# Performance work log

Measured on AMD Instinct MI355X. Metric: run time of the kernel, lower is better.

The kernel has to match this reference:

```python
import math
import jax, jax.numpy as jnp
import numpy as np

B, N, D = 4, 2048, 512
H, DV, DO = 8, 64, 512


def setup_inputs() -> dict:
    key = jax.random.key(0)
    ks = jax.random.split(key, 8)
    def xavier(k, shape, fan_in, fan_out):
        a = math.sqrt(6.0 / (fan_in + fan_out))
        return jax.random.uniform(k, shape, jnp.float32, -a, a)
    return {
        "query": jax.random.normal(ks[0], (B, N, D), jnp.float32),
        "key": jax.random.normal(ks[1], (B, N, D), jnp.float32),
        "value": jax.random.normal(ks[2], (B, N, D), jnp.float32),
        "attn_mask": jax.random.randint(ks[3], (N, N), 0, 2, jnp.int32),
        "Wq": xavier(ks[4], (H, D, D), D, D),
        "Wk": xavier(ks[5], (H, D, D), D, D),
        "Wv": xavier(ks[6], (H, D, DV), D, DV),
        "Wo": xavier(ks[7], (H * DV, DO), H * DV, DO),
    }


def reference(query, key, value, attn_mask, Wq, Wk, Wv, Wo):
    b, n, d = query.shape
    h, dv = Wv.shape[0], Wv.shape[2]
    # per-head projections: [b, h, n, d] / [b, h, n, dv]
    Q = jnp.einsum('bnd,hde->bhne', query, Wq)
    K = jnp.einsum('bnd,hde->bhne', key, Wk)
    V = jnp.einsum('bnd,hdv->bhnv', value, Wv)
    # multiplicative mask (1: do not attend -> zeroed score), scaled by sqrt(d)
    keep = (1.0 - attn_mask.astype(jnp.float32))[None, None]  # [1,1,n,n]
    QK = jnp.einsum('bhne,bhme->bhnm', Q, K) * keep / math.sqrt(d)
    attn_weights = QK  # linear_attention=True: skip softmax
    QKV = jnp.einsum('bhnm,bhmv->bhnv', attn_weights, V)  # [b,h,n,dv]
    out = QKV.transpose(0, 2, 1, 3).reshape(b, n, h * dv) @ Wo  # [b,n,do]
    return (out, attn_weights)
```

## Files before the change

### kernel.cpp

```cpp
#include <hip/hip_runtime.h>
#include <hip/hip_bf16.h>

#define DEVFN __device__ __forceinline__

constexpr int Bb = 4, Nn = 2048, Dd = 512, Hh = 8, DVv = 64, DOo = 512;

typedef short short8 __attribute__((ext_vector_type(8)));
typedef float f32x4 __attribute__((ext_vector_type(4)));

typedef __attribute__((address_space(1))) void GV;
typedef __attribute__((address_space(3))) void LV;

DEVFN unsigned short f32_bf16(float f) {
  unsigned u = __builtin_bit_cast(unsigned, f);
  u += 0x7fffu + ((u >> 16) & 1u);
  return (unsigned short)(u >> 16);
}

DEVFN void barrier_raw() {
  asm volatile("" ::: "memory");
  __builtin_amdgcn_s_barrier();
  asm volatile("" ::: "memory");
}

template<int Nv> DEVFN void wait_vmcnt() {
  if constexpr (Nv == 0)      asm volatile("s_waitcnt vmcnt(0)"  ::: "memory");
  else if constexpr (Nv == 6) asm volatile("s_waitcnt vmcnt(6)"  ::: "memory");
  else if constexpr (Nv == 8) asm volatile("s_waitcnt vmcnt(8)"  ::: "memory");
  else static_assert(Nv == 0 || Nv == 6 || Nv == 8, "bad vmcnt");
}
DEVFN void wait_lgkm0() { asm volatile("s_waitcnt lgkmcnt(0)" ::: "memory"); }

template<int ROWBYTES, int TOTAL>
DEVFN void stage_tile(const char* g, int strideBytes, char* lds, int tid) {
#pragma unroll
  for (int off = 0; off < TOTAL; off += 4096) {
    int o   = off + tid * 16;
    int row = o / ROWBYTES;
    int blk = (o >> 4) & ((ROWBYTES >> 4) - 1);
    int sb  = blk ^ (row & 7);
    const char* src = g + (size_t)row * strideBytes + (sb << 4);
    __builtin_amdgcn_global_load_lds((GV*)src, (LV*)(lds + o), 16, 0, 0);
  }
}

template<int ROWBYTES>
DEVFN short8 frag_ld(const char* lds, int row, int kbyte) {
  int blk = kbyte >> 4;
  int sb  = blk ^ (row & 7);
  return *(const short8*)(lds + row * ROWBYTES + (sb << 4));
}

DEVFN f32x4 mfma16(short8 a, short8 b, f32x4 c) {
  return __builtin_amdgcn_mfma_f32_16x16x32_bf16(a, b, c, 0, 0, 0);
}


__global__ void cvt_f32_bf16_kernel(const float* __restrict__ in,
                                    unsigned short* __restrict__ out, int n4) {
  int i = blockIdx.x * blockDim.x + threadIdx.x;
  if (i < n4) {
    float4 v = ((const float4*)in)[i];
    ushort4 o;
    o.x = f32_bf16(v.x); o.y = f32_bf16(v.y);
    o.z = f32_bf16(v.z); o.w = f32_bf16(v.w);
    ((ushort4*)out)[i] = o;
  }
}

__global__ void mask_prep_kernel(const int* __restrict__ m,
                                 unsigned short* __restrict__ ms, int n4) {
  int i = blockIdx.x * blockDim.x + threadIdx.x;
  if (i < n4) {
    int4 v = ((const int4*)m)[i];
    ushort4 o;
    o.x = v.x ? 0 : 0x3f80; o.y = v.y ? 0 : 0x3f80;
    o.z = v.z ? 0 : 0x3f80; o.w = v.w ? 0 : 0x3f80;
    ((ushort4*)ms)[i] = o;
  }
}

__global__ void transpose_w_kernel(const float* __restrict__ in,
                                   unsigned short* __restrict__ out, int R, int C) {
  __shared__ float t[32][33];
  int g = blockIdx.z;
  int c0 = blockIdx.x * 32, r0 = blockIdx.y * 32;
  const float* ip = in + (size_t)g * R * C;
  unsigned short* op = out + (size_t)g * R * C;
#pragma unroll
  for (int i = threadIdx.y; i < 32; i += 8)
    t[i][threadIdx.x] = ip[(size_t)(r0 + i) * C + c0 + threadIdx.x];
  __syncthreads();
#pragma unroll
  for (int i = threadIdx.y; i < 32; i += 8)
    op[(size_t)(c0 + i) * R + r0 + threadIdx.x] = f32_bf16(t[threadIdx.x][i]);
}

__global__ void transpose_u16_kernel(const unsigned short* __restrict__ in,
                                     unsigned short* __restrict__ out, int R, int C) {
  __shared__ unsigned short t[32][33];
  int g = blockIdx.z;
  int c0 = blockIdx.x * 32, r0 = blockIdx.y * 32;
  const unsigned short* ip = in + (size_t)g * R * C;
  unsigned short* op = out + (size_t)g * R * C;
#pragma unroll
  for (int i = threadIdx.y; i < 32; i += 8)
    t[i][threadIdx.x] = ip[(size_t)(r0 + i) * C + c0 + threadIdx.x];
  __syncthreads();
#pragma unroll
  for (int i = threadIdx.y; i < 32; i += 8)
    op[(size_t)(c0 + i) * R + r0 + threadIdx.x] = t[threadIdx.x][i];
}


template<int NCG, bool OUTF32>
__global__ __launch_bounds__(256)
void gemm_nt_kernel(const unsigned short* __restrict__ A,
                    const unsigned short* __restrict__ BtAll,
                    void* __restrict__ Cb, int HeadsOut, int Ncols) {
  constexpr int BN = NCG * 32;
  constexpr int NL = 4 + BN / 32;
  __shared__ alignas(16) char As[2][16384];
  __shared__ alignas(16) char Bs[2][BN * 128];
  int tid = threadIdx.x, lane = tid & 63;
  int w = tid >> 6, wr = w >> 1, wc = w & 1;
  int tM = blockIdx.x, tN = blockIdx.y, h = blockIdx.z;
  const char* Ab  = (const char*)A + ((size_t)tM * 128) * 1024;
  const char* Btb = (const char*)BtAll + ((size_t)h * Ncols + tN * BN) * 1024;

  f32x4 acc[4][NCG] = {};

  stage_tile<128, 16384>(Ab, 1024, As[0], tid);
  stage_tile<128, BN * 128>(Btb, 1024, Bs[0], tid);
#pragma unroll
  for (int kk = 0; kk < 8; ++kk) {
    int cur = kk & 1;
    if (kk < 7) {
      stage_tile<128, 16384>(Ab + (kk + 1) * 128, 1024, As[cur ^ 1], tid);
      stage_tile<128, BN * 128>(Btb + (kk + 1) * 128, 1024, Bs[cur ^ 1], tid);
      wait_vmcnt<NL>();
    } else {
      wait_vmcnt<0>();
    }
    barrier_raw();
#pragma unroll
    for (int c = 0; c < 2; ++c) {
      short8 af[4], bf[NCG];
#pragma unroll
      for (int rg = 0; rg < 4; ++rg)
        af[rg] = frag_ld<128>(As[cur], wr * 64 + rg * 16 + (lane & 15),
                              c * 64 + (lane >> 4) * 16);
#pragma unroll
      for (int cg = 0; cg < NCG; ++cg)
        bf[cg] = frag_ld<128>(Bs[cur], wc * (NCG * 16) + cg * 16 + (lane & 15),
                              c * 64 + (lane >> 4) * 16);
#pragma unroll
      for (int rg = 0; rg < 4; ++rg)
#pragma unroll
        for (int cg = 0; cg < NCG; ++cg)
          acc[rg][cg] = mfma16(af[rg], bf[cg], acc[rg][cg]);
    }
    barrier_raw();
  }

#pragma unroll
  for (int rg = 0; rg < 4; ++rg)
#pragma unroll
    for (int cg = 0; cg < NCG; ++cg)
#pragma unroll
      for (int r = 0; r < 4; ++r) {
        int grow = tM * 128 + wr * 64 + rg * 16 + (lane >> 4) * 4 + r;
        int col  = tN * BN + wc * (NCG * 16) + cg * 16 + (lane & 15);
        size_t orow = ((size_t)(grow >> 11) * HeadsOut + h) * 2048 + (grow & 2047);
        if constexpr (OUTF32)
          ((float*)Cb)[orow * Ncols + col] = acc[rg][cg][r];
        else
          ((unsigned short*)Cb)[orow * Ncols + col] = f32_bf16(acc[rg][cg][r]);
      }
}


__global__ __launch_bounds__(256)
void qk_attn_kernel(const unsigned short* __restrict__ Qb,
                    const unsigned short* __restrict__ Kb,
                    const unsigned short* __restrict__ ms,
                    float* __restrict__ attn_out, int bh0) {
  __shared__ alignas(16) char As[2][16384];
  __shared__ alignas(16) char Bs[2][16384];
  int tid = threadIdx.x, lane = tid & 63;
  int w = tid >> 6, wr = w >> 1, wc = w & 1;
  int fid = blockIdx.x;
  int orig = (fid & 7) * 256 + (fid >> 3);
  int tM = orig & 15, tN = (orig >> 4) & 15, bh = bh0 + (orig >> 8);

  const char* Ab  = (const char*)Qb + ((size_t)bh * Nn + tM * 128) * 1024;
  const char* Btb = (const char*)Kb + ((size_t)bh * Nn + tN * 128) * 1024;
  const float scale = 0.044194173824159216f;

  f32x4 acc[4][4] = {};

  stage_tile<128, 16384>(Ab, 1024, As[0], tid);
  stage_tile<128, 16384>(Btb, 1024, Bs[0], tid);
#pragma unroll
  for (int kk = 0; kk < 8; ++kk) {
    int cur = kk & 1;
    if (kk < 7) {
      stage_tile<128, 16384>(Ab + (kk + 1) * 128, 1024, As[cur ^ 1], tid);
      stage_tile<128, 16384>(Btb + (kk + 1) * 128, 1024, Bs[cur ^ 1], tid);
      wait_vmcnt<8>();
    } else {
      wait_vmcnt<0>();
    }
    barrier_raw();
#pragma unroll
    for (int c = 0; c < 2; ++c) {
      short8 af[4], bf[4];
#pragma unroll
      for (int rg = 0; rg < 4; ++rg)
        af[rg] = frag_ld<128>(As[cur], wr * 64 + rg * 16 + (lane & 15),
                              c * 64 + (lane >> 4) * 16);
#pragma unroll
      for (int cg = 0; cg < 4; ++cg)
        bf[cg] = frag_ld<128>(Bs[cur], wc * 64 + cg * 16 + (lane & 15),
                              c * 64 + (lane >> 4) * 16);
#pragma unroll
      for (int rg = 0; rg < 4; ++rg)
#pragma unroll
        for (int cg = 0; cg < 4; ++cg)
          acc[rg][cg] = mfma16(af[rg], bf[cg], acc[rg][cg]);
    }
    barrier_raw();
  }

#pragma unroll
  for (int rg = 0; rg < 4; ++rg)
#pragma unroll
    for (int cg = 0; cg < 4; ++cg)
#pragma unroll
      for (int r = 0; r < 4; ++r) {
        int rowL = wr * 64 + rg * 16 + (lane >> 4) * 4 + r;
        int colL = wc * 64 + cg * 16 + (lane & 15);
        int qrow = tM * 128 + rowL, kcol = tN * 128 + colL;
        unsigned short kv = ms[(size_t)qrow * Nn + kcol];
        float keep = __builtin_bit_cast(float, (unsigned)kv << 16);
        attn_out[((size_t)bh * Nn + qrow) * Nn + kcol] =
            acc[rg][cg][r] * scale * keep;
      }
}


__global__ __launch_bounds__(256)
void pv_kernel(const float* __restrict__ attn,
               const unsigned short* __restrict__ VbT,
               unsigned short* __restrict__ QKV, int bh0) {
  __shared__ alignas(16) char As[2][8192];
  __shared__ alignas(16) char Bs[2][8192];
  int tid = threadIdx.x, lane = tid & 63;
  int w = tid >> 6, wr = w >> 1, wc = w & 1;
  int tM = blockIdx.x, bh = bh0 + blockIdx.y;
  int b = bh >> 3, h = bh & 7;

  int arow = tid >> 2, aseg = tid & 3;
  const float* Ag = attn + ((size_t)bh * Nn + (size_t)tM * 64 + arow) * Nn
                    + aseg * 16;
  const char* Btb = (const char*)VbT + (size_t)bh * DVv * Nn * 2;

  f32x4 acc[2][2] = {};

  auto packA = [&](float4 ar[4], char* dst) {
    short8 s0, s1;
#pragma unroll
    for (int e = 0; e < 4; ++e) {
      s0[e]     = (short)f32_bf16(ar[0][e]);
      s0[e + 4] = (short)f32_bf16(ar[1][e]);
      s1[e]     = (short)f32_bf16(ar[2][e]);
      s1[e + 4] = (short)f32_bf16(ar[3][e]);
    }
    int b0 = (aseg * 2) ^ (arow & 7), b1 = (aseg * 2 + 1) ^ (arow & 7);
    *(short8*)(dst + arow * 128 + (b0 << 4)) = s0;
    *(short8*)(dst + arow * 128 + (b1 << 4)) = s1;
  };

  {
    float4 ar[4];
#pragma unroll
    for (int i = 0; i < 4; ++i) ar[i] = ((const float4*)Ag)[i];
    stage_tile<128, 8192>(Btb, Nn * 2, Bs[0], tid);
    wait_vmcnt<0>();
    packA(ar, As[0]);
    wait_lgkm0();
    barrier_raw();
  }

#pragma unroll 2
  for (int kk = 0; kk < 32; ++kk) {
    int cur = kk & 1;
    float4 ar[4];
    if (kk < 31) {
      const float* an = Ag + (kk + 1) * 64;
#pragma unroll
      for (int i = 0; i < 4; ++i) ar[i] = ((const float4*)an)[i];
      stage_tile<128, 8192>(Btb + (kk + 1) * 128, Nn * 2, Bs[cur ^ 1], tid);
    }
#pragma unroll
    for (int c = 0; c < 2; ++c) {
      short8 af[2], bf2[2];
#pragma unroll
      for (int rg = 0; rg < 2; ++rg)
        af[rg] = frag_ld<128>(As[cur], wr * 32 + rg * 16 + (lane & 15),
                              c * 64 + (lane >> 4) * 16);
#pragma unroll
      for (int cg = 0; cg < 2; ++cg)
        bf2[cg] = frag_ld<128>(Bs[cur], wc * 32 + cg * 16 + (lane & 15),
                               c * 64 + (lane >> 4) * 16);
#pragma unroll
      for (int rg = 0; rg < 2; ++rg)
#pragma unroll
        for (int cg = 0; cg < 2; ++cg)
          acc[rg][cg] = mfma16(af[rg], bf2[cg], acc[rg][cg]);
    }
    if (kk < 31) {
      wait_vmcnt<0>();
      packA(ar, As[cur ^ 1]);
      wait_lgkm0();
    }
    barrier_raw();
  }

#pragma unroll
  for (int rg = 0; rg < 2; ++rg)
#pragma unroll
    for (int cg = 0; cg < 2; ++cg)
#pragma unroll
      for (int r = 0; r < 4; ++r) {
        int rowL = wr * 32 + rg * 16 + (lane >> 4) * 4 + r;
        int colL = wc * 32 + cg * 16 + (lane & 15);
        size_t grow = (size_t)tM * 64 + rowL;
        QKV[((size_t)b * Nn + grow) * (Hh * DVv) + h * DVv + colL] =
            f32_bf16(acc[rg][cg][r]);
      }
}


extern "C" void kernel_launch(void* const* d_in, const int* in_sizes, int n_in,
                              void* d_out, int out_size, void* d_ws, size_t ws_size,
                              hipStream_t stream) {
  const float* q    = (const float*)d_in[0];
  const float* k    = (const float*)d_in[1];
  const float* v    = (const float*)d_in[2];
  const int*   mask = (const int*)d_in[3];
  const float* Wq   = (const float*)d_in[4];
  const float* Wk   = (const float*)d_in[5];
  const float* Wv   = (const float*)d_in[6];
  const float* Wo   = (const float*)d_in[7];

  char* ws = (char*)d_ws;
  size_t off = 0;
  auto alloc = [&](size_t bytes) {
    char* p = ws + off;
    off += (bytes + 255) & ~(size_t)255;
    return p;
  };
  unsigned short* WqT  = (unsigned short*)alloc((size_t)Hh * Dd * Dd * 2);
  unsigned short* WkT  = (unsigned short*)alloc((size_t)Hh * Dd * Dd * 2);
  unsigned short* WvT  = (unsigned short*)alloc((size_t)Hh * DVv * Dd * 2);
  unsigned short* WoT  = (unsigned short*)alloc((size_t)DOo * Hh * DVv * 2);
  unsigned short* Xq   = (unsigned short*)alloc((size_t)Bb * Nn * Dd * 2);
  unsigned short* Xk   = (unsigned short*)alloc((size_t)Bb * Nn * Dd * 2);
  unsigned short* Xv   = (unsigned short*)alloc((size_t)Bb * Nn * Dd * 2);
  unsigned short* Qb   = (unsigned short*)alloc((size_t)Bb * Hh * Nn * Dd * 2);
  unsigned short* Kb   = (unsigned short*)alloc((size_t)Bb * Hh * Nn * Dd * 2);
  unsigned short* Vb   = (unsigned short*)alloc((size_t)Bb * Hh * Nn * DVv * 2);
  unsigned short* VbT  = (unsigned short*)alloc((size_t)Bb * Hh * DVv * Nn * 2);
  unsigned short* QKVb = (unsigned short*)alloc((size_t)Bb * Nn * Hh * DVv * 2);
  unsigned short* Ms   = (unsigned short*)alloc((size_t)Nn * Nn * 2);

  int n4 = Bb * Nn * Dd / 4;
  cvt_f32_bf16_kernel<<<dim3(n4 / 256), dim3(256), 0, stream>>>(q, Xq, n4);
  cvt_f32_bf16_kernel<<<dim3(n4 / 256), dim3(256), 0, stream>>>(k, Xk, n4);
  cvt_f32_bf16_kernel<<<dim3(n4 / 256), dim3(256), 0, stream>>>(v, Xv, n4);
  mask_prep_kernel<<<dim3(Nn * Nn / 4 / 256), dim3(256), 0, stream>>>(mask, Ms, Nn * Nn / 4);

  transpose_w_kernel<<<dim3(Dd / 32, Dd / 32, Hh), dim3(32, 8), 0, stream>>>(Wq, WqT, Dd, Dd);
  transpose_w_kernel<<<dim3(Dd / 32, Dd / 32, Hh), dim3(32, 8), 0, stream>>>(Wk, WkT, Dd, Dd);
  transpose_w_kernel<<<dim3(DVv / 32, Dd / 32, Hh), dim3(32, 8), 0, stream>>>(Wv, WvT, Dd, DVv);
  transpose_w_kernel<<<dim3(DOo / 32, (Hh * DVv) / 32, 1), dim3(32, 8), 0, stream>>>(Wo, WoT, Hh * DVv, DOo);

  gemm_nt_kernel<4, false><<<dim3(64, 4, Hh), dim3(256), 0, stream>>>(Xq, WqT, Qb, Hh, Dd);
  gemm_nt_kernel<4, false><<<dim3(64, 4, Hh), dim3(256), 0, stream>>>(Xk, WkT, Kb, Hh, Dd);
  gemm_nt_kernel<2, false><<<dim3(64, 1, Hh), dim3(256), 0, stream>>>(Xv, WvT, Vb, Hh, DVv);

  transpose_u16_kernel<<<dim3(DVv / 32, Nn / 32, Bb * Hh), dim3(32, 8), 0, stream>>>(Vb, VbT, Nn, DVv);

  float* outp  = (float*)d_out;
  float* attnp = outp + (size_t)Bb * Nn * DOo;

  for (int c = 0; c < 4; ++c) {
    qk_attn_kernel<<<dim3(2048), dim3(256), 0, stream>>>(Qb, Kb, Ms, attnp, c * 8);
    pv_kernel<<<dim3(32, 8), dim3(256), 0, stream>>>(attnp, VbT, QKVb, c * 8);
  }

  gemm_nt_kernel<4, true><<<dim3(64, 4, 1), dim3(256), 0, stream>>>(QKVb, WoT, outp, 1, DOo);

  (void)in_sizes; (void)n_in; (void)out_size; (void)ws_size;
}
```

Before: 605.3 us.

## Add 256x256-tile 512-thread GEMM with 4-stage pipeline for QK and projections

Adds a new gemm256 kernel that uses 256x256 output tiles, 8 waves and a 4-buffer LDS pipeline with 64-byte K slices, loads prefetched three steps ahead, and raised wave priority around the MFMA block. It replaces the Q/K projection GEMMs and the QK^T attention-score kernel. It also collapses the four chunked qk/pv launches into one QK launch followed by one PV launch over all batch-heads. The larger tiles are meant to improve operand reuse and hide memory latency. In exchange the kernel holds a 128-entry accumulator array per thread, uses 128KB of LDS, and loses the L2 locality the chunked schedule gave PV when it read the attention matrix.

```diff
diff --git a/kernel.cpp b/kernel.cpp
--- a/kernel.cpp
+++ b/kernel.cpp
@@ -25,20 +25,22 @@
 
 template<int Nv> DEVFN void wait_vmcnt() {
   if constexpr (Nv == 0)      asm volatile("s_waitcnt vmcnt(0)"  ::: "memory");
+  else if constexpr (Nv == 4) asm volatile("s_waitcnt vmcnt(4)"  ::: "memory");
   else if constexpr (Nv == 6) asm volatile("s_waitcnt vmcnt(6)"  ::: "memory");
   else if constexpr (Nv == 8) asm volatile("s_waitcnt vmcnt(8)"  ::: "memory");
-  else static_assert(Nv == 0 || Nv == 6 || Nv == 8, "bad vmcnt");
+  else static_assert(Nv == 0 || Nv == 4 || Nv == 6 || Nv == 8, "bad vmcnt");
 }
 DEVFN void wait_lgkm0() { asm volatile("s_waitcnt lgkmcnt(0)" ::: "memory"); }
 
-template<int ROWBYTES, int TOTAL>
+template<int ROWBYTES, int TOTAL, int NTHR = 256>
 DEVFN void stage_tile(const char* g, int strideBytes, char* lds, int tid) {
-#pragma unroll
-  for (int off = 0; off < TOTAL; off += 4096) {
+  constexpr int MASK = (ROWBYTES >> 4) - 1;
+#pragma unroll
+  for (int off = 0; off < TOTAL; off += NTHR * 16) {
     int o   = off + tid * 16;
     int row = o / ROWBYTES;
-    int blk = (o >> 4) & ((ROWBYTES >> 4) - 1);
-    int sb  = blk ^ (row & 7);
+    int blk = (o >> 4) & MASK;
+    int sb  = blk ^ (row & MASK & 7);
     const char* src = g + (size_t)row * strideBytes + (sb << 4);
     __builtin_amdgcn_global_load_lds((GV*)src, (LV*)(lds + o), 16, 0, 0);
   }
@@ -46,8 +48,9 @@
 
 template<int ROWBYTES>
 DEVFN short8 frag_ld(const char* lds, int row, int kbyte) {
+  constexpr int MASK = (ROWBYTES >> 4) - 1;
   int blk = kbyte >> 4;
-  int sb  = blk ^ (row & 7);
+  int sb  = blk ^ (row & MASK & 7);
   return *(const short8*)(lds + row * ROWBYTES + (sb << 4));
 }
 
@@ -110,6 +113,86 @@
 #pragma unroll
   for (int i = threadIdx.y; i < 32; i += 8)
     op[(size_t)(c0 + i) * R + r0 + threadIdx.x] = t[threadIdx.x][i];
+}
+
+
+template<int NTM, int NTN, int NG, int EPI>
+__global__ __launch_bounds__(512, 2)
+void gemm256_kernel(const char* __restrict__ A, long sAg,
+                    const char* __restrict__ Bt, long sBg,
+                    void* __restrict__ C, const unsigned short* __restrict__ ms) {
+  __shared__ alignas(16) char Asl[4][16384];
+  __shared__ alignas(16) char Bsl[4][16384];
+  int tid = threadIdx.x, lane = tid & 63;
+  int w = tid >> 6, wr = w >> 2, wc = w & 3;
+
+  constexpr int TOT = NTM * NTN * NG;
+  int fid = blockIdx.x;
+  int swz = (fid & 7) * (TOT / 8) + (fid >> 3);
+  int g = swz / (NTM * NTN), rem = swz % (NTM * NTN);
+  int tM = rem % NTM, tN = rem / NTM;
+
+  const char* Ag = A + (size_t)g * sAg + (size_t)tM * 256 * 1024;
+  const char* Bg = Bt + (size_t)g * sBg + (size_t)tN * 256 * 1024;
+
+  f32x4 acc[8][4] = {};
+
+#pragma unroll
+  for (int u = 0; u < 3; ++u) {
+    stage_tile<64, 16384, 512>(Ag + u * 64, 1024, Asl[u], tid);
+    stage_tile<64, 16384, 512>(Bg + u * 64, 1024, Bsl[u], tid);
+  }
+
+#pragma unroll
+  for (int u = 0; u < 16; ++u) {
+    if (u <= 13)      wait_vmcnt<8>();
+    else if (u == 14) wait_vmcnt<4>();
+    else              wait_vmcnt<0>();
+    barrier_raw();
+    short8 af[8], bfr[4];
+#pragma unroll
+    for (int rg = 0; rg < 8; ++rg)
+      af[rg] = frag_ld<64>(Asl[u & 3], wr * 128 + rg * 16 + (lane & 15),
+                           (lane >> 4) * 16);
+#pragma unroll
+    for (int cg = 0; cg < 4; ++cg)
+      bfr[cg] = frag_ld<64>(Bsl[u & 3], wc * 64 + cg * 16 + (lane & 15),
+                            (lane >> 4) * 16);
+    if (u < 13) {
+      stage_tile<64, 16384, 512>(Ag + (u + 3) * 64, 1024, Asl[(u + 3) & 3], tid);
+      stage_tile<64, 16384, 512>(Bg + (u + 3) * 64, 1024, Bsl[(u + 3) & 3], tid);
+    }
+    __builtin_amdgcn_s_setprio(1);
+#pragma unroll
+    for (int rg = 0; rg < 8; ++rg)
+#pragma unroll
+      for (int cg = 0; cg < 4; ++cg)
+        acc[rg][cg] = mfma16(af[rg], bfr[cg], acc[rg][cg]);
+    __builtin_amdgcn_s_setprio(0);
+    barrier_raw();
+  }
+
+  const float scale = 0.044194173824159216f;
+#pragma unroll
+  for (int rg = 0; rg < 8; ++rg)
+#pragma unroll
+    for (int cg = 0; cg < 4; ++cg)
+#pragma unroll
+      for (int r = 0; r < 4; ++r) {
+        int rowL = wr * 128 + rg * 16 + (lane >> 4) * 4 + r;
+        int colL = wc * 64 + cg * 16 + (lane & 15);
+        int grow = tM * 256 + rowL;
+        int col  = tN * 256 + colL;
+        if constexpr (EPI == 0) {
+          size_t orow = ((size_t)(grow >> 11) * Hh + g) * 2048 + (grow & 2047);
+          ((unsigned short*)C)[orow * 512 + col] = f32_bf16(acc[rg][cg][r]);
+        } else {
+          unsigned short kv = ms[(size_t)grow * Nn + col];
+          float keep = __builtin_bit_cast(float, (unsigned)kv << 16);
+          ((float*)C)[((size_t)g * Nn + grow) * Nn + col] =
+              acc[rg][cg][r] * scale * keep;
+        }
+      }
 }
 
 
@@ -138,7 +221,7 @@
     if (kk < 7) {
       stage_tile<128, 16384>(Ab + (kk + 1) * 128, 1024, As[cur ^ 1], tid);
       stage_tile<128, BN * 128>(Btb + (kk + 1) * 128, 1024, Bs[cur ^ 1], tid);
-      wait_vmcnt<NL>();
+      wait_vmcnt<NL == 8 ? 8 : 6>();
     } else {
       wait_vmcnt<0>();
     }
@@ -181,83 +264,14 @@
 
 
 __global__ __launch_bounds__(256)
-void qk_attn_kernel(const unsigned short* __restrict__ Qb,
-                    const unsigned short* __restrict__ Kb,
-                    const unsigned short* __restrict__ ms,
-                    float* __restrict__ attn_out, int bh0) {
-  __shared__ alignas(16) char As[2][16384];
-  __shared__ alignas(16) char Bs[2][16384];
-  int tid = threadIdx.x, lane = tid & 63;
-  int w = tid >> 6, wr = w >> 1, wc = w & 1;
-  int fid = blockIdx.x;
-  int orig = (fid & 7) * 256 + (fid >> 3);
-  int tM = orig & 15, tN = (orig >> 4) & 15, bh = bh0 + (orig >> 8);
-
-  const char* Ab  = (const char*)Qb + ((size_t)bh * Nn + tM * 128) * 1024;
-  const char* Btb = (const char*)Kb + ((size_t)bh * Nn + tN * 128) * 1024;
-  const float scale = 0.044194173824159216f;
-
-  f32x4 acc[4][4] = {};
-
-  stage_tile<128, 16384>(Ab, 1024, As[0], tid);
-  stage_tile<128, 16384>(Btb, 1024, Bs[0], tid);
-#pragma unroll
-  for (int kk = 0; kk < 8; ++kk) {
-    int cur = kk & 1;
-    if (kk < 7) {
-      stage_tile<128, 16384>(Ab + (kk + 1) * 128, 1024, As[cur ^ 1], tid);
-      stage_tile<128, 16384>(Btb + (kk + 1) * 128, 1024, Bs[cur ^ 1], tid);
-      wait_vmcnt<8>();
-    } else {
-      wait_vmcnt<0>();
-    }
-    barrier_raw();
-#pragma unroll
-    for (int c = 0; c < 2; ++c) {
-      short8 af[4], bf[4];
-#pragma unroll
-      for (int rg = 0; rg < 4; ++rg)
-        af[rg] = frag_ld<128>(As[cur], wr * 64 + rg * 16 + (lane & 15),
-                              c * 64 + (lane >> 4) * 16);
-#pragma unroll
-      for (int cg = 0; cg < 4; ++cg)
-        bf[cg] = frag_ld<128>(Bs[cur], wc * 64 + cg * 16 + (lane & 15),
-                              c * 64 + (lane >> 4) * 16);
-#pragma unroll
-      for (int rg = 0; rg < 4; ++rg)
-#pragma unroll
-        for (int cg = 0; cg < 4; ++cg)
-          acc[rg][cg] = mfma16(af[rg], bf[cg], acc[rg][cg]);
-    }
-    barrier_raw();
-  }
-
-#pragma unroll
-  for (int rg = 0; rg < 4; ++rg)
-#pragma unroll
-    for (int cg = 0; cg < 4; ++cg)
-#pragma unroll
-      for (int r = 0; r < 4; ++r) {
-        int rowL = wr * 64 + rg * 16 + (lane >> 4) * 4 + r;
-        int colL = wc * 64 + cg * 16 + (lane & 15);
-        int qrow = tM * 128 + rowL, kcol = tN * 128 + colL;
-        unsigned short kv = ms[(size_t)qrow * Nn + kcol];
-        float keep = __builtin_bit_cast(float, (unsigned)kv << 16);
-        attn_out[((size_t)bh * Nn + qrow) * Nn + kcol] =
-            acc[rg][cg][r] * scale * keep;
-      }
-}
-
-
-__global__ __launch_bounds__(256)
 void pv_kernel(const float* __restrict__ attn,
                const unsigned short* __restrict__ VbT,
-               unsigned short* __restrict__ QKV, int bh0) {
+               unsigned short* __restrict__ QKV) {
   __shared__ alignas(16) char As[2][8192];
   __shared__ alignas(16) char Bs[2][8192];
   int tid = threadIdx.x, lane = tid & 63;
   int w = tid >> 6, wr = w >> 1, wc = w & 1;
-  int tM = blockIdx.x, bh = bh0 + blockIdx.y;
+  int tM = blockIdx.x, bh = blockIdx.y;
   int b = bh >> 3, h = bh & 7;
 
   int arow = tid >> 2, aseg = tid & 3;
@@ -386,8 +400,10 @@
   transpose_w_kernel<<<dim3(DVv / 32, Dd / 32, Hh), dim3(32, 8), 0, stream>>>(Wv, WvT, Dd, DVv);
   transpose_w_kernel<<<dim3(DOo / 32, (Hh * DVv) / 32, 1), dim3(32, 8), 0, stream>>>(Wo, WoT, Hh * DVv, DOo);
 
-  gemm_nt_kernel<4, false><<<dim3(64, 4, Hh), dim3(256), 0, stream>>>(Xq, WqT, Qb, Hh, Dd);
-  gemm_nt_kernel<4, false><<<dim3(64, 4, Hh), dim3(256), 0, stream>>>(Xk, WkT, Kb, Hh, Dd);
+  gemm256_kernel<32, 2, 8, 0><<<dim3(512), dim3(512), 0, stream>>>(
+      (const char*)Xq, 0L, (const char*)WqT, (long)Dd * Dd * 2, Qb, nullptr);
+  gemm256_kernel<32, 2, 8, 0><<<dim3(512), dim3(512), 0, stream>>>(
+      (const char*)Xk, 0L, (const char*)WkT, (long)Dd * Dd * 2, Kb, nullptr);
   gemm_nt_kernel<2, false><<<dim3(64, 1, Hh), dim3(256), 0, stream>>>(Xv, WvT, Vb, Hh, DVv);
 
   transpose_u16_kernel<<<dim3(DVv / 32, Nn / 32, Bb * Hh), dim3(32, 8), 0, stream>>>(Vb, VbT, Nn, DVv);
@@ -395,10 +411,11 @@
   float* outp  = (float*)d_out;
   float* attnp = outp + (size_t)Bb * Nn * DOo;
 
-  for (int c = 0; c < 4; ++c) {
-    qk_attn_kernel<<<dim3(2048), dim3(256), 0, stream>>>(Qb, Kb, Ms, attnp, c * 8);
-    pv_kernel<<<dim3(32, 8), dim3(256), 0, stream>>>(attnp, VbT, QKVb, c * 8);
-  }
+  gemm256_kernel<8, 8, 32, 1><<<dim3(2048), dim3(512), 0, stream>>>(
+      (const char*)Qb, (long)Nn * Dd * 2, (const char*)Kb, (long)Nn * Dd * 2,
+      attnp, Ms);
+
+  pv_kernel<<<dim3(32, 32), dim3(256), 0, stream>>>(attnp, VbT, QKVb);
 
   gemm_nt_kernel<4, true><<<dim3(64, 4, 1), dim3(256), 0, stream>>>(QKVb, WoT, outp, 1, DOo);
 
```

Measured after the change: 609.4 us. Within noise of the previous version (+0.7%).

## Fuse prep launches, write V transposed, emit bf16 scores for a new PV GEMM

Applied to the files above, without the earlier changes.

Merges the three fp32→bf16 conversions into one launch and the four weight transposes into one launch. The V projection epilogue now writes V already transposed, which removes the separate transpose kernel. The QK kernel runs as a single launch over all batch-heads and, when workspace allows, also writes a bf16 copy of the scores. A new pv2 kernel streams that copy through LDS with async loads instead of re-reading and converting the fp32 attention. This trades an extra 256MB bf16 write and workspace space for halving the PV read traffic and dropping the per-chunk launch loop, and falls back to the old path if the workspace is too small.

```diff
diff --git a/kernel.cpp b/kernel.cpp
--- a/kernel.cpp
+++ b/kernel.cpp
@@ -31,14 +31,15 @@
 }
 DEVFN void wait_lgkm0() { asm volatile("s_waitcnt lgkmcnt(0)" ::: "memory"); }
 
-template<int ROWBYTES, int TOTAL>
+template<int ROWBYTES, int TOTAL, int NTHR = 256>
 DEVFN void stage_tile(const char* g, int strideBytes, char* lds, int tid) {
-#pragma unroll
-  for (int off = 0; off < TOTAL; off += 4096) {
+  constexpr int MASK = (ROWBYTES >> 4) - 1;
+#pragma unroll
+  for (int off = 0; off < TOTAL; off += NTHR * 16) {
     int o   = off + tid * 16;
     int row = o / ROWBYTES;
-    int blk = (o >> 4) & ((ROWBYTES >> 4) - 1);
-    int sb  = blk ^ (row & 7);
+    int blk = (o >> 4) & MASK;
+    int sb  = blk ^ (row & MASK & 7);
     const char* src = g + (size_t)row * strideBytes + (sb << 4);
     __builtin_amdgcn_global_load_lds((GV*)src, (LV*)(lds + o), 16, 0, 0);
   }
@@ -46,8 +47,9 @@
 
 template<int ROWBYTES>
 DEVFN short8 frag_ld(const char* lds, int row, int kbyte) {
+  constexpr int MASK = (ROWBYTES >> 4) - 1;
   int blk = kbyte >> 4;
-  int sb  = blk ^ (row & 7);
+  int sb  = blk ^ (row & MASK & 7);
   return *(const short8*)(lds + row * ROWBYTES + (sb << 4));
 }
 
@@ -56,16 +58,20 @@
 }
 
 
-__global__ void cvt_f32_bf16_kernel(const float* __restrict__ in,
-                                    unsigned short* __restrict__ out, int n4) {
+__global__ void cvt3_kernel(const float* __restrict__ q, const float* __restrict__ k,
+                            const float* __restrict__ v,
+                            unsigned short* __restrict__ Xq,
+                            unsigned short* __restrict__ Xk,
+                            unsigned short* __restrict__ Xv, int n4) {
   int i = blockIdx.x * blockDim.x + threadIdx.x;
-  if (i < n4) {
-    float4 v = ((const float4*)in)[i];
-    ushort4 o;
-    o.x = f32_bf16(v.x); o.y = f32_bf16(v.y);
-    o.z = f32_bf16(v.z); o.w = f32_bf16(v.w);
-    ((ushort4*)out)[i] = o;
-  }
+  if (i >= n4) return;
+  const float* in = blockIdx.y == 0 ? q : (blockIdx.y == 1 ? k : v);
+  unsigned short* out = blockIdx.y == 0 ? Xq : (blockIdx.y == 1 ? Xk : Xv);
+  float4 val = ((const float4*)in)[i];
+  ushort4 o;
+  o.x = f32_bf16(val.x); o.y = f32_bf16(val.y);
+  o.z = f32_bf16(val.z); o.w = f32_bf16(val.w);
+  ((ushort4*)out)[i] = o;
 }
 
 __global__ void mask_prep_kernel(const int* __restrict__ m,
@@ -80,13 +86,23 @@
   }
 }
 
-__global__ void transpose_w_kernel(const float* __restrict__ in,
-                                   unsigned short* __restrict__ out, int R, int C) {
+__global__ void transpose_wall_kernel(const float* __restrict__ Wq,
+                                      const float* __restrict__ Wk,
+                                      const float* __restrict__ Wv,
+                                      const float* __restrict__ Wo,
+                                      unsigned short* __restrict__ WqT,
+                                      unsigned short* __restrict__ WkT,
+                                      unsigned short* __restrict__ WvT,
+                                      unsigned short* __restrict__ WoT) {
   __shared__ float t[32][33];
-  int g = blockIdx.z;
+  int z = blockIdx.z;
+  const float* ip; unsigned short* op; int R, C;
+  if (z < 8)       { ip = Wq + (size_t)z * Dd * Dd;        op = WqT + (size_t)z * Dd * Dd;        R = Dd; C = Dd; }
+  else if (z < 16) { ip = Wk + (size_t)(z - 8) * Dd * Dd;  op = WkT + (size_t)(z - 8) * Dd * Dd;  R = Dd; C = Dd; }
+  else if (z < 24) { ip = Wv + (size_t)(z - 16) * Dd * DVv; op = WvT + (size_t)(z - 16) * Dd * DVv; R = Dd; C = DVv; }
+  else             { ip = Wo; op = WoT; R = Hh * DVv; C = DOo; }
   int c0 = blockIdx.x * 32, r0 = blockIdx.y * 32;
-  const float* ip = in + (size_t)g * R * C;
-  unsigned short* op = out + (size_t)g * R * C;
+  if (c0 >= C || r0 >= R) return;
 #pragma unroll
   for (int i = threadIdx.y; i < 32; i += 8)
     t[i][threadIdx.x] = ip[(size_t)(r0 + i) * C + c0 + threadIdx.x];
@@ -96,24 +112,8 @@
     op[(size_t)(c0 + i) * R + r0 + threadIdx.x] = f32_bf16(t[threadIdx.x][i]);
 }
 
-__global__ void transpose_u16_kernel(const unsigned short* __restrict__ in,
-                                     unsigned short* __restrict__ out, int R, int C) {
-  __shared__ unsigned short t[32][33];
-  int g = blockIdx.z;
-  int c0 = blockIdx.x * 32, r0 = blockIdx.y * 32;
-  const unsigned short* ip = in + (size_t)g * R * C;
-  unsigned short* op = out + (size_t)g * R * C;
-#pragma unroll
-  for (int i = threadIdx.y; i < 32; i += 8)
-    t[i][threadIdx.x] = ip[(size_t)(r0 + i) * C + c0 + threadIdx.x];
-  __syncthreads();
-#pragma unroll
-  for (int i = threadIdx.y; i < 32; i += 8)
-    op[(size_t)(c0 + i) * R + r0 + threadIdx.x] = t[threadIdx.x][i];
-}
-
-
-template<int NCG, bool OUTF32>
+
+template<int NCG, int EPI>
 __global__ __launch_bounds__(256)
 void gemm_nt_kernel(const unsigned short* __restrict__ A,
                     const unsigned short* __restrict__ BtAll,
@@ -138,7 +138,7 @@
     if (kk < 7) {
       stage_tile<128, 16384>(Ab + (kk + 1) * 128, 1024, As[cur ^ 1], tid);
       stage_tile<128, BN * 128>(Btb + (kk + 1) * 128, 1024, Bs[cur ^ 1], tid);
-      wait_vmcnt<NL>();
+      wait_vmcnt<NL == 8 ? 8 : 6>();
     } else {
       wait_vmcnt<0>();
     }
@@ -166,17 +166,29 @@
 #pragma unroll
   for (int rg = 0; rg < 4; ++rg)
 #pragma unroll
-    for (int cg = 0; cg < NCG; ++cg)
-#pragma unroll
-      for (int r = 0; r < 4; ++r) {
-        int grow = tM * 128 + wr * 64 + rg * 16 + (lane >> 4) * 4 + r;
-        int col  = tN * BN + wc * (NCG * 16) + cg * 16 + (lane & 15);
-        size_t orow = ((size_t)(grow >> 11) * HeadsOut + h) * 2048 + (grow & 2047);
-        if constexpr (OUTF32)
-          ((float*)Cb)[orow * Ncols + col] = acc[rg][cg][r];
-        else
-          ((unsigned short*)Cb)[orow * Ncols + col] = f32_bf16(acc[rg][cg][r]);
+    for (int cg = 0; cg < NCG; ++cg) {
+      if constexpr (EPI == 2) {
+        int grow0 = tM * 128 + wr * 64 + rg * 16 + (lane >> 4) * 4;
+        int col   = tN * BN + wc * (NCG * 16) + cg * 16 + (lane & 15);
+        int bq = grow0 >> 11, n0 = grow0 & 2047;
+        ushort4 o;
+        o.x = f32_bf16(acc[rg][cg][0]); o.y = f32_bf16(acc[rg][cg][1]);
+        o.z = f32_bf16(acc[rg][cg][2]); o.w = f32_bf16(acc[rg][cg][3]);
+        *(ushort4*)&((unsigned short*)Cb)[
+            (((size_t)bq * Hh + h) * DVv + col) * 2048 + n0] = o;
+      } else {
+#pragma unroll
+        for (int r = 0; r < 4; ++r) {
+          int grow = tM * 128 + wr * 64 + rg * 16 + (lane >> 4) * 4 + r;
+          int col  = tN * BN + wc * (NCG * 16) + cg * 16 + (lane & 15);
+          size_t orow = ((size_t)(grow >> 11) * HeadsOut + h) * 2048 + (grow & 2047);
+          if constexpr (EPI == 1)
+            ((float*)Cb)[orow * Ncols + col] = acc[rg][cg][r];
+          else
+            ((unsigned short*)Cb)[orow * Ncols + col] = f32_bf16(acc[rg][cg][r]);
+        }
       }
+    }
 }
 
 
@@ -184,14 +196,15 @@
 void qk_attn_kernel(const unsigned short* __restrict__ Qb,
                     const unsigned short* __restrict__ Kb,
                     const unsigned short* __restrict__ ms,
-                    float* __restrict__ attn_out, int bh0) {
+                    float* __restrict__ attn_out,
+                    unsigned short* __restrict__ Sbf) {
   __shared__ alignas(16) char As[2][16384];
   __shared__ alignas(16) char Bs[2][16384];
   int tid = threadIdx.x, lane = tid & 63;
   int w = tid >> 6, wr = w >> 1, wc = w & 1;
   int fid = blockIdx.x;
-  int orig = (fid & 7) * 256 + (fid >> 3);
-  int tM = orig & 15, tN = (orig >> 4) & 15, bh = bh0 + (orig >> 8);
+  int orig = (fid & 7) * 1024 + (fid >> 3);
+  int tM = orig & 15, tN = (orig >> 4) & 15, bh = orig >> 8;
 
   const char* Ab  = (const char*)Qb + ((size_t)bh * Nn + tM * 128) * 1024;
   const char* Btb = (const char*)Kb + ((size_t)bh * Nn + tN * 128) * 1024;
@@ -243,8 +256,73 @@
         int qrow = tM * 128 + rowL, kcol = tN * 128 + colL;
         unsigned short kv = ms[(size_t)qrow * Nn + kcol];
         float keep = __builtin_bit_cast(float, (unsigned)kv << 16);
-        attn_out[((size_t)bh * Nn + qrow) * Nn + kcol] =
-            acc[rg][cg][r] * scale * keep;
+        float vv = acc[rg][cg][r] * scale * keep;
+        size_t idx = ((size_t)bh * Nn + qrow) * Nn + kcol;
+        attn_out[idx] = vv;
+        if (Sbf) Sbf[idx] = f32_bf16(vv);
+      }
+}
+
+
+__global__ __launch_bounds__(256)
+void pv2_kernel(const unsigned short* __restrict__ Sb,
+                const unsigned short* __restrict__ VbT,
+                unsigned short* __restrict__ QKV) {
+  __shared__ alignas(16) char As[2][16384];
+  __shared__ alignas(16) char Bs[2][8192];
+  int tid = threadIdx.x, lane = tid & 63;
+  int w = tid >> 6, wr = w >> 1, wc = w & 1;
+  int tM = blockIdx.x, bh = blockIdx.y;
+  int b = bh >> 3, h = bh & 7;
+  const char* Ab  = (const char*)Sb + ((size_t)bh * Nn + tM * 128) * (Nn * 2);
+  const char* Btb = (const char*)VbT + (size_t)bh * DVv * Nn * 2;
+
+  f32x4 acc[4][2] = {};
+
+  stage_tile<128, 16384>(Ab, Nn * 2, As[0], tid);
+  stage_tile<128, 8192>(Btb, Nn * 2, Bs[0], tid);
+#pragma unroll 2
+  for (int kk = 0; kk < 32; ++kk) {
+    int cur = kk & 1;
+    if (kk < 31) {
+      stage_tile<128, 16384>(Ab + (kk + 1) * 128, Nn * 2, As[cur ^ 1], tid);
+      stage_tile<128, 8192>(Btb + (kk + 1) * 128, Nn * 2, Bs[cur ^ 1], tid);
+      wait_vmcnt<6>();
+    } else {
+      wait_vmcnt<0>();
+    }
+    barrier_raw();
+#pragma unroll
+    for (int c = 0; c < 2; ++c) {
+      short8 af[4], bf2[2];
+#pragma unroll
+      for (int rg = 0; rg < 4; ++rg)
+        af[rg] = frag_ld<128>(As[cur], wr * 64 + rg * 16 + (lane & 15),
+                              c * 64 + (lane >> 4) * 16);
+#pragma unroll
+      for (int cg = 0; cg < 2; ++cg)
+        bf2[cg] = frag_ld<128>(Bs[cur], wc * 32 + cg * 16 + (lane & 15),
+                               c * 64 + (lane >> 4) * 16);
+#pragma unroll
+      for (int rg = 0; rg < 4; ++rg)
+#pragma unroll
+        for (int cg = 0; cg < 2; ++cg)
+          acc[rg][cg] = mfma16(af[rg], bf2[cg], acc[rg][cg]);
+    }
+    barrier_raw();
+  }
+
+#pragma unroll
+  for (int rg = 0; rg < 4; ++rg)
+#pragma unroll
+    for (int cg = 0; cg < 2; ++cg)
+#pragma unroll
+      for (int r = 0; r < 4; ++r) {
+        int rowL = wr * 64 + rg * 16 + (lane >> 4) * 4 + r;
+        int colL = wc * 32 + cg * 16 + (lane & 15);
+        size_t grow = (size_t)tM * 128 + rowL;
+        QKV[((size_t)b * Nn + grow) * (Hh * DVv) + h * DVv + colL] =
+            f32_bf16(acc[rg][cg][r]);
       }
 }
 
@@ -252,12 +330,12 @@
 __global__ __launch_bounds__(256)
 void pv_kernel(const float* __restrict__ attn,
                const unsigned short* __restrict__ VbT,
-               unsigned short* __restrict__ QKV, int bh0) {
+               unsigned short* __restrict__ QKV) {
   __shared__ alignas(16) char As[2][8192];
   __shared__ alignas(16) char Bs[2][8192];
   int tid = threadIdx.x, lane = tid & 63;
   int w = tid >> 6, wr = w >> 1, wc = w & 1;
-  int tM = blockIdx.x, bh = bh0 + blockIdx.y;
+  int tM = blockIdx.x, bh = blockIdx.y;
   int b = bh >> 3, h = bh & 7;
 
   int arow = tid >> 2, aseg = tid & 3;
@@ -370,37 +448,34 @@
   unsigned short* Xv   = (unsigned short*)alloc((size_t)Bb * Nn * Dd * 2);
   unsigned short* Qb   = (unsigned short*)alloc((size_t)Bb * Hh * Nn * Dd * 2);
   unsigned short* Kb   = (unsigned short*)alloc((size_t)Bb * Hh * Nn * Dd * 2);
-  unsigned short* Vb   = (unsigned short*)alloc((size_t)Bb * Hh * Nn * DVv * 2);
   unsigned short* VbT  = (unsigned short*)alloc((size_t)Bb * Hh * DVv * Nn * 2);
   unsigned short* QKVb = (unsigned short*)alloc((size_t)Bb * Nn * Hh * DVv * 2);
   unsigned short* Ms   = (unsigned short*)alloc((size_t)Nn * Nn * 2);
+  size_t sbf_bytes = (size_t)Bb * Hh * Nn * Nn * 2;
+  bool use_sbf = (off + sbf_bytes) <= ws_size;
+  unsigned short* Sbf = use_sbf ? (unsigned short*)alloc(sbf_bytes) : nullptr;
 
   int n4 = Bb * Nn * Dd / 4;
-  cvt_f32_bf16_kernel<<<dim3(n4 / 256), dim3(256), 0, stream>>>(q, Xq, n4);
-  cvt_f32_bf16_kernel<<<dim3(n4 / 256), dim3(256), 0, stream>>>(k, Xk, n4);
-  cvt_f32_bf16_kernel<<<dim3(n4 / 256), dim3(256), 0, stream>>>(v, Xv, n4);
+  cvt3_kernel<<<dim3(n4 / 256, 3), dim3(256), 0, stream>>>(q, k, v, Xq, Xk, Xv, n4);
   mask_prep_kernel<<<dim3(Nn * Nn / 4 / 256), dim3(256), 0, stream>>>(mask, Ms, Nn * Nn / 4);
-
-  transpose_w_kernel<<<dim3(Dd / 32, Dd / 32, Hh), dim3(32, 8), 0, stream>>>(Wq, WqT, Dd, Dd);
-  transpose_w_kernel<<<dim3(Dd / 32, Dd / 32, Hh), dim3(32, 8), 0, stream>>>(Wk, WkT, Dd, Dd);
-  transpose_w_kernel<<<dim3(DVv / 32, Dd / 32, Hh), dim3(32, 8), 0, stream>>>(Wv, WvT, Dd, DVv);
-  transpose_w_kernel<<<dim3(DOo / 32, (Hh * DVv) / 32, 1), dim3(32, 8), 0, stream>>>(Wo, WoT, Hh * DVv, DOo);
-
-  gemm_nt_kernel<4, false><<<dim3(64, 4, Hh), dim3(256), 0, stream>>>(Xq, WqT, Qb, Hh, Dd);
-  gemm_nt_kernel<4, false><<<dim3(64, 4, Hh), dim3(256), 0, stream>>>(Xk, WkT, Kb, Hh, Dd);
-  gemm_nt_kernel<2, false><<<dim3(64, 1, Hh), dim3(256), 0, stream>>>(Xv, WvT, Vb, Hh, DVv);
-
-  transpose_u16_kernel<<<dim3(DVv / 32, Nn / 32, Bb * Hh), dim3(32, 8), 0, stream>>>(Vb, VbT, Nn, DVv);
+  transpose_wall_kernel<<<dim3(16, 16, 25), dim3(32, 8), 0, stream>>>(
+      Wq, Wk, Wv, Wo, WqT, WkT, WvT, WoT);
+
+  gemm_nt_kernel<4, 0><<<dim3(64, 4, Hh), dim3(256), 0, stream>>>(Xq, WqT, Qb, Hh, Dd);
+  gemm_nt_kernel<4, 0><<<dim3(64, 4, Hh), dim3(256), 0, stream>>>(Xk, WkT, Kb, Hh, Dd);
+  gemm_nt_kernel<2, 2><<<dim3(64, 1, Hh), dim3(256), 0, stream>>>(Xv, WvT, VbT, Hh, DVv);
 
   float* outp  = (float*)d_out;
   float* attnp = outp + (size_t)Bb * Nn * DOo;
 
-  for (int c = 0; c < 4; ++c) {
-    qk_attn_kernel<<<dim3(2048), dim3(256), 0, stream>>>(Qb, Kb, Ms, attnp, c * 8);
-    pv_kernel<<<dim3(32, 8), dim3(256), 0, stream>>>(attnp, VbT, QKVb, c * 8);
-  }
-
-  gemm_nt_kernel<4, true><<<dim3(64, 4, 1), dim3(256), 0, stream>>>(QKVb, WoT, outp, 1, DOo);
-
-  (void)in_sizes; (void)n_in; (void)out_size; (void)ws_size;
-}
+  qk_attn_kernel<<<dim3(8192), dim3(256), 0, stream>>>(Qb, Kb, Ms, attnp, Sbf);
+
+  if (use_sbf)
+    pv2_kernel<<<dim3(16, 32), dim3(256), 0, stream>>>(Sbf, VbT, QKVb);
+  else
+    pv_kernel<<<dim3(32, 32), dim3(256), 0, stream>>>(attnp, VbT, QKVb);
+
+  gemm_nt_kernel<4, 1><<<dim3(64, 4, 1), dim3(256), 0, stream>>>(QKVb, WoT, outp, 1, DOo);
+
+  (void)in_sizes; (void)n_in; (void)out_size;
+}
```

After: 802.2 us. 1.33x slower.
